# Kernel optimization log

Measured on AMD Instinct MI355X. Metric: run time of the kernel, lower is better.

The kernel has to match this reference:

```python
import jax, jax.numpy as jnp
import numpy as np

N_QUBITS = 4
N_LAYERS = 2
BATCH = 524288


def _apply_1q(state, U, wire, batched):
    """Apply a 2x2 gate U on `wire`. state: [B,2,2,2,2]; U: [B,2,2] if batched else [2,2]."""
    ax = wire + 1
    s = jnp.moveaxis(state, ax, 1)
    if batched:
        s = jnp.einsum('bij,bj...->bi...', U, s)
    else:
        s = jnp.einsum('ij,bj...->bi...', U, s)
    return jnp.moveaxis(s, 1, ax)


def _apply_cnot(state, control, target):
    cax, tax = control + 1, target + 1
    s0 = jnp.take(state, 0, axis=cax)
    s1 = jnp.take(state, 1, axis=cax)
    t_ax = tax - 1 if tax > cax else tax  # target axis after removing control axis
    s1 = jnp.flip(s1, axis=t_ax)
    return jnp.stack([s0, s1], axis=cax)


def _circuit(x, weight):
    B = x.shape[0]
    # Angle encoding: RY(tanh(x_i) * pi) per wire (per-sample angles)
    theta = jnp.tanh(x) * jnp.pi  # [B, 4]
    state = jnp.zeros((B,) + (2,) * N_QUBITS, jnp.complex64)
    state = state.at[(slice(None),) + (0,) * N_QUBITS].set(1.0)
    for q in range(N_QUBITS):
        h = theta[:, q] * 0.5
        c, s = jnp.cos(h), jnp.sin(h)
        Ury = jnp.stack([jnp.stack([c, -s], -1), jnp.stack([s, c], -1)], -2).astype(jnp.complex64)  # [B,2,2]
        state = _apply_1q(state, Ury, q, batched=True)
    for layer in range(N_LAYERS):
        for q in range(N_QUBITS):
            hy = weight[layer, q, 0] * 0.5
            cy, sy = jnp.cos(hy), jnp.sin(hy)
            Uy = jnp.stack([jnp.stack([cy, -sy]), jnp.stack([sy, cy])]).astype(jnp.complex64)
            state = _apply_1q(state, Uy, q, batched=False)
            hz = weight[layer, q, 1] * 0.5
            ez = jnp.exp(-1j * hz.astype(jnp.complex64))
            z0 = jnp.zeros((), jnp.complex64)
            Uz = jnp.stack([jnp.stack([ez, z0]), jnp.stack([z0, jnp.conj(ez)])])
            state = _apply_1q(state, Uz, q, batched=False)
        for q in range(N_QUBITS):
            state = _apply_cnot(state, q, (q + 1) % N_QUBITS)
    # <Z_i> = P(bit_i = 0) - P(bit_i = 1)
    probs = jnp.abs(state) ** 2  # [B,2,2,2,2] float32
    outs = []
    for q in range(N_QUBITS):
        other_axes = tuple(a for a in range(1, N_QUBITS + 1) if a != q + 1)
        marg = probs.sum(other_axes)  # [B,2]
        outs.append(marg[:, 0] - marg[:, 1])
    return jnp.stack(outs, axis=-1).astype(jnp.float32)  # [B,4]


def setup_inputs() -> dict:
    key = jax.random.key(0)
    kx, kw = jax.random.split(key)
    x = jax.random.normal(kx, (BATCH, N_QUBITS), dtype=jnp.float32)
    weight = jax.random.normal(kw, (N_LAYERS, N_QUBITS, 2), dtype=jnp.float32) * 0.1
    return {"x": x, "weight": weight}


def reference(x, weight):
    return _circuit(x, weight)
```

## Files before the change

kernel.cpp:

```cpp
#include <hip/hip_runtime.h>
#include <math.h>


#define HALF_PI_F 1.57079632679489661923f

__global__ __launch_bounds__(256) void build_C(
    const float* __restrict__ weight,
    float* __restrict__ C)
{
    __shared__ float cw[16], sw[16];
    __shared__ float Ur[16][16], Ui[16][16];
    __shared__ float A[4][16][16];

    if (threadIdx.x < 16) {
        float h = 0.5f * weight[threadIdx.x];
        __sincosf(h, &sw[threadIdx.x], &cw[threadIdx.x]);
    }
    __syncthreads();

    if (threadIdx.x < 16) {
        int col = threadIdx.x;
        float re[16], im[16];
        #pragma unroll
        for (int i = 0; i < 16; ++i) { re[i] = 0.f; im[i] = 0.f; }
        re[col] = 1.f;

        #pragma unroll
        for (int layer = 0; layer < 2; ++layer) {
            #pragma unroll
            for (int q = 0; q < 4; ++q) {
                float cy = cw[layer*8 + q*2 + 0];
                float sy = sw[layer*8 + q*2 + 0];
                float cz = cw[layer*8 + q*2 + 1];
                float sz = sw[layer*8 + q*2 + 1];
                int st = 8 >> q;
                #pragma unroll
                for (int i = 0; i < 16; ++i) {
                    if (i & st) continue;
                    int j = i | st;
                    float r0 = re[i], r1 = re[j], i0 = im[i], i1 = im[j];
                    float nr0 = cy*r0 - sy*r1;
                    float nr1 = sy*r0 + cy*r1;
                    float ni0 = cy*i0 - sy*i1;
                    float ni1 = sy*i0 + cy*i1;
                    re[i] = nr0*cz + ni0*sz;
                    im[i] = ni0*cz - nr0*sz;
                    re[j] = nr1*cz - ni1*sz;
                    im[j] = ni1*cz + nr1*sz;
                }
            }
            #pragma unroll
            for (int q = 0; q < 4; ++q) {
                int cb = 8 >> q;
                int tb = 8 >> ((q + 1) & 3);
                #pragma unroll
                for (int i = 0; i < 16; ++i) {
                    if ((i & cb) && !(i & tb)) {
                        int j = i | tb;
                        float tr = re[i]; re[i] = re[j]; re[j] = tr;
                        float ti = im[i]; im[i] = im[j]; im[j] = ti;
                    }
                }
            }
        }
        #pragma unroll
        for (int i = 0; i < 16; ++i) { Ur[i][col] = re[i]; Ui[i][col] = im[i]; }
    }
    __syncthreads();

    for (int e = threadIdx.x; e < 1024; e += 256) {
        int q = e >> 8, j = (e >> 4) & 15, k = e & 15;
        float sum = 0.f;
        for (int i = 0; i < 16; ++i) {
            float t = Ur[i][j]*Ur[i][k] + Ui[i][j]*Ui[i][k];
            sum += (i & (8 >> q)) ? -t : t;
        }
        A[q][j][k] = sum;
    }
    __syncthreads();

    for (int e = threadIdx.x; e < 400; e += 256) {
        int q = e / 100, pi = (e / 10) % 10, qi = e % 10;
        const int pu[10] = {0,0,0,0,1,1,1,2,2,3};
        const int pv[10] = {0,1,2,3,1,2,3,2,3,3};
        int u = pu[pi], v = pv[pi], r = pu[qi], s = pv[qi];
        float sum = 0.f;
        int a1s[2] = {u, v}, a2s[2] = {v, u};
        int b1s[2] = {r, s}, b2s[2] = {s, r};
        int na = (u == v) ? 1 : 2;
        int nb = (r == s) ? 1 : 2;
        for (int ia = 0; ia < na; ++ia)
            for (int ib = 0; ib < nb; ++ib)
                sum += A[q][a1s[ia]*4 + b1s[ib]][a2s[ia]*4 + b2s[ib]];
        C[e] = sum;
    }
}

__global__ __launch_bounds__(256) void qmain(
    const float* __restrict__ x,
    const float* __restrict__ C,
    float* __restrict__ out,
    int B)
{
    int tid = blockIdx.x * blockDim.x + threadIdx.x;
    if (tid >= B) return;

    float4 xv = reinterpret_cast<const float4*>(x)[tid];
    float xs[4] = {xv.x, xv.y, xv.z, xv.w};

    float c[4], s[4];
    #pragma unroll
    for (int q = 0; q < 4; ++q) {
        float e = __expf(2.f * xs[q]);
        float t = 1.f - __fdividef(2.f, e + 1.f);
        __sincosf(t * HALF_PI_F, &s[q], &c[q]);
    }

    float a4[4] = {c[0]*c[1], c[0]*s[1], s[0]*c[1], s[0]*s[1]};
    float b4[4] = {c[2]*c[3], c[2]*s[3], s[2]*c[3], s[2]*s[3]};

    const int pu[10] = {0,0,0,0,1,1,1,2,2,3};
    const int pv[10] = {0,1,2,3,1,2,3,2,3,3};
    float P[10], Q[10];
    #pragma unroll
    for (int i2 = 0; i2 < 10; ++i2) {
        P[i2] = a4[pu[i2]] * a4[pv[i2]];
        Q[i2] = b4[pu[i2]] * b4[pv[i2]];
    }

    float z[4];
    #pragma unroll
    for (int q = 0; q < 4; ++q) {
        float zq = 0.f;
        #pragma unroll
        for (int pi = 0; pi < 10; ++pi) {
            float t = 0.f;
            #pragma unroll
            for (int qi = 0; qi < 10; ++qi)
                t = fmaf(C[q*100 + pi*10 + qi], Q[qi], t);
            zq = fmaf(P[pi], t, zq);
        }
        z[q] = zq;
    }

    float4 o = {z[0], z[1], z[2], z[3]};
    reinterpret_cast<float4*>(out)[tid] = o;
}

extern "C" void kernel_launch(void* const* d_in, const int* in_sizes, int n_in,
                              void* d_out, int out_size, void* d_ws, size_t ws_size,
                              hipStream_t stream) {
    const float* x = (const float*)d_in[0];
    const float* w = (const float*)d_in[1];
    float* out = (float*)d_out;
    float* C = (float*)d_ws;
    int B = in_sizes[0] / 4;

    build_C<<<1, 256, 0, stream>>>(w, C);
    int block = 256;
    int grid = (B + block - 1) / block;
    qmain<<<grid, block, 0, stream>>>(x, C, out, B);
}
```

Baseline: 73.79 us.

## Fuse C-matrix build into main kernel, two samples per thread with packed math

```diff
diff --git a/kernel.cpp b/kernel.cpp
--- a/kernel.cpp
+++ b/kernel.cpp
@@ -4,71 +4,89 @@
 
 #define HALF_PI_F 1.57079632679489661923f
 
-__global__ __launch_bounds__(256) void build_C(
+typedef float f32x2 __attribute__((ext_vector_type(2)));
+
+__global__ __launch_bounds__(256) void qfused(
+    const float* __restrict__ x,
     const float* __restrict__ weight,
-    float* __restrict__ C)
+    float* __restrict__ out,
+    int B)
 {
     __shared__ float cw[16], sw[16];
     __shared__ float Ur[16][16], Ui[16][16];
     __shared__ float A[4][16][16];
+    __shared__ float4 C4[10][10];
 
-    if (threadIdx.x < 16) {
-        float h = 0.5f * weight[threadIdx.x];
-        __sincosf(h, &sw[threadIdx.x], &cw[threadIdx.x]);
+    const int tid = threadIdx.x;
+    const int s0 = blockIdx.x * 512 + tid;
+    const int s1 = s0 + 256;
+
+    float4 xv0 = (s0 < B) ? reinterpret_cast<const float4*>(x)[s0]
+                          : float4{0.f, 0.f, 0.f, 0.f};
+    float4 xv1 = (s1 < B) ? reinterpret_cast<const float4*>(x)[s1]
+                          : float4{0.f, 0.f, 0.f, 0.f};
+
+    if (tid < 16) {
+        float h = 0.5f * weight[tid];
+        __sincosf(h, &sw[tid], &cw[tid]);
     }
     __syncthreads();
 
-    if (threadIdx.x < 16) {
-        int col = threadIdx.x;
-        float re[16], im[16];
-        #pragma unroll
-        for (int i = 0; i < 16; ++i) { re[i] = 0.f; im[i] = 0.f; }
-        re[col] = 1.f;
+    {
+        const int wbase = (blockIdx.x & 3) * 64;
+        if (tid >= wbase && tid < wbase + 16) {
+            const int col = tid - wbase;
+            float re[16], im[16];
+            #pragma unroll
+            for (int i = 0; i < 16; ++i) { re[i] = 0.f; im[i] = 0.f; }
+            re[col] = 1.f;
 
-        #pragma unroll
-        for (int layer = 0; layer < 2; ++layer) {
             #pragma unroll
-            for (int q = 0; q < 4; ++q) {
-                float cy = cw[layer*8 + q*2 + 0];
-                float sy = sw[layer*8 + q*2 + 0];
-                float cz = cw[layer*8 + q*2 + 1];
-                float sz = sw[layer*8 + q*2 + 1];
-                int st = 8 >> q;
+            for (int layer = 0; layer < 2; ++layer) {
                 #pragma unroll
-                for (int i = 0; i < 16; ++i) {
-                    if (i & st) continue;
-                    int j = i | st;
-                    float r0 = re[i], r1 = re[j], i0 = im[i], i1 = im[j];
-                    float nr0 = cy*r0 - sy*r1;
-                    float nr1 = sy*r0 + cy*r1;
-                    float ni0 = cy*i0 - sy*i1;
-                    float ni1 = sy*i0 + cy*i1;
-                    re[i] = nr0*cz + ni0*sz;
-                    im[i] = ni0*cz - nr0*sz;
-                    re[j] = nr1*cz - ni1*sz;
-                    im[j] = ni1*cz + nr1*sz;
+                for (int q = 0; q < 4; ++q) {
+                    float cy = cw[layer*8 + q*2 + 0];
+                    float sy = sw[layer*8 + q*2 + 0];
+                    float cz = cw[layer*8 + q*2 + 1];
+                    float sz = sw[layer*8 + q*2 + 1];
+                    int st = 8 >> q;
+                    #pragma unroll
+                    for (int i = 0; i < 16; ++i) {
+                        if (i & st) continue;
+                        int j = i | st;
+                        float r0 = re[i], r1 = re[j], i0 = im[i], i1 = im[j];
+                        float nr0 = cy*r0 - sy*r1;
+                        float nr1 = sy*r0 + cy*r1;
+                        float ni0 = cy*i0 - sy*i1;
+                        float ni1 = sy*i0 + cy*i1;
+                        re[i] = nr0*cz + ni0*sz;
+                        im[i] = ni0*cz - nr0*sz;
+                        re[j] = nr1*cz - ni1*sz;
+                        im[j] = ni1*cz + nr1*sz;
+                    }
+                }
+                #pragma unroll
+                for (int q = 0; q < 4; ++q) {
+                    int cb = 8 >> q;
+                    int tb = 8 >> ((q + 1) & 3);
+                    #pragma unroll
+                    for (int i = 0; i < 16; ++i) {
+                        if ((i & cb) && !(i & tb)) {
+                            int j = i | tb;
+                            float tr = re[i]; re[i] = re[j]; re[j] = tr;
+                            float ti = im[i]; im[i] = im[j]; im[j] = ti;
+                        }
+                    }
                 }
             }
             #pragma unroll
-            for (int q = 0; q < 4; ++q) {
-                int cb = 8 >> q;
-                int tb = 8 >> ((q + 1) & 3);
-                #pragma unroll
-                for (int i = 0; i < 16; ++i) {
-                    if ((i & cb) && !(i & tb)) {
-                        int j = i | tb;
-                        float tr = re[i]; re[i] = re[j]; re[j] = tr;
-                        float ti = im[i]; im[i] = im[j]; im[j] = ti;
-                    }
-                }
-            }
+            for (int i = 0; i < 16; ++i) { Ur[i][col] = re[i]; Ui[i][col] = im[i]; }
         }
-        #pragma unroll
-        for (int i = 0; i < 16; ++i) { Ur[i][col] = re[i]; Ui[i][col] = im[i]; }
     }
     __syncthreads();
 
-    for (int e = threadIdx.x; e < 1024; e += 256) {
+    #pragma unroll
+    for (int e = tid; e < 1024; e += 256) {
         int q = e >> 8, j = (e >> 4) & 15, k = e & 15;
         float sum = 0.f;
         for (int i = 0; i < 16; ++i) {
@@ -79,72 +97,81 @@
     }
     __syncthreads();
 
-    for (int e = threadIdx.x; e < 400; e += 256) {
-        int q = e / 100, pi = (e / 10) % 10, qi = e % 10;
+    if (tid < 100) {
         const int pu[10] = {0,0,0,0,1,1,1,2,2,3};
         const int pv[10] = {0,1,2,3,1,2,3,2,3,3};
-        int u = pu[pi], v = pv[pi], r = pu[qi], s = pv[qi];
-        float sum = 0.f;
+        int pi = tid / 10, qi = tid % 10;
+        int u = pu[pi], v = pv[pi], r = pu[qi], sI = pv[qi];
         int a1s[2] = {u, v}, a2s[2] = {v, u};
-        int b1s[2] = {r, s}, b2s[2] = {s, r};
+        int b1s[2] = {r, sI}, b2s[2] = {sI, r};
         int na = (u == v) ? 1 : 2;
-        int nb = (r == s) ? 1 : 2;
+        int nb = (r == sI) ? 1 : 2;
+        float acc[4] = {0.f, 0.f, 0.f, 0.f};
         for (int ia = 0; ia < na; ++ia)
-            for (int ib = 0; ib < nb; ++ib)
-                sum += A[q][a1s[ia]*4 + b1s[ib]][a2s[ia]*4 + b2s[ib]];
-        C[e] = sum;
+            for (int ib = 0; ib < nb; ++ib) {
+                int j = a1s[ia]*4 + b1s[ib];
+                int k = a2s[ia]*4 + b2s[ib];
+                #pragma unroll
+                for (int q = 0; q < 4; ++q) acc[q] += A[q][j][k];
+            }
+        C4[pi][qi] = float4{acc[0], acc[1], acc[2], acc[3]};
     }
-}
-
-__global__ __launch_bounds__(256) void qmain(
-    const float* __restrict__ x,
-    const float* __restrict__ C,
-    float* __restrict__ out,
-    int B)
-{
-    int tid = blockIdx.x * blockDim.x + threadIdx.x;
-    if (tid >= B) return;
-
-    float4 xv = reinterpret_cast<const float4*>(x)[tid];
-    float xs[4] = {xv.x, xv.y, xv.z, xv.w};
-
-    float c[4], s[4];
-    #pragma unroll
-    for (int q = 0; q < 4; ++q) {
-        float e = __expf(2.f * xs[q]);
-        float t = 1.f - __fdividef(2.f, e + 1.f);
-        __sincosf(t * HALF_PI_F, &s[q], &c[q]);
-    }
-
-    float a4[4] = {c[0]*c[1], c[0]*s[1], s[0]*c[1], s[0]*s[1]};
-    float b4[4] = {c[2]*c[3], c[2]*s[3], s[2]*c[3], s[2]*s[3]};
+    __syncthreads();
 
     const int pu[10] = {0,0,0,0,1,1,1,2,2,3};
     const int pv[10] = {0,1,2,3,1,2,3,2,3,3};
-    float P[10], Q[10];
-    #pragma unroll
-    for (int i2 = 0; i2 < 10; ++i2) {
-        P[i2] = a4[pu[i2]] * a4[pv[i2]];
-        Q[i2] = b4[pu[i2]] * b4[pv[i2]];
+
+    float P0[10], Q0[10], P1[10], Q1[10];
+    {
+        float xs[8] = {xv0.x, xv0.y, xv0.z, xv0.w, xv1.x, xv1.y, xv1.z, xv1.w};
+        float c[8], s[8];
+        #pragma unroll
+        for (int q = 0; q < 8; ++q) {
+            float e = __expf(2.f * xs[q]);
+            float t = 1.f - __fdividef(2.f, e + 1.f);
+            __sincosf(t * HALF_PI_F, &s[q], &c[q]);
+        }
+        float a0[4] = {c[0]*c[1], c[0]*s[1], s[0]*c[1], s[0]*s[1]};
+        float b0[4] = {c[2]*c[3], c[2]*s[3], s[2]*c[3], s[2]*s[3]};
+        float a1[4] = {c[4]*c[5], c[4]*s[5], s[4]*c[5], s[4]*s[5]};
+        float b1[4] = {c[6]*c[7], c[6]*s[7], s[6]*c[7], s[6]*s[7]};
+        #pragma unroll
+        for (int i2 = 0; i2 < 10; ++i2) {
+            P0[i2] = a0[pu[i2]] * a0[pv[i2]];
+            Q0[i2] = b0[pu[i2]] * b0[pv[i2]];
+            P1[i2] = a1[pu[i2]] * a1[pv[i2]];
+            Q1[i2] = b1[pu[i2]] * b1[pv[i2]];
+        }
     }
 
-    float z[4];
+    f32x2 z01_0 = {0.f, 0.f}, z23_0 = {0.f, 0.f};
+    f32x2 z01_1 = {0.f, 0.f}, z23_1 = {0.f, 0.f};
     #pragma unroll
-    for (int q = 0; q < 4; ++q) {
-        float zq = 0.f;
+    for (int pi = 0; pi < 10; ++pi) {
+        f32x2 t01_0 = {0.f, 0.f}, t23_0 = {0.f, 0.f};
+        f32x2 t01_1 = {0.f, 0.f}, t23_1 = {0.f, 0.f};
         #pragma unroll
-        for (int pi = 0; pi < 10; ++pi) {
-            float t = 0.f;
-            #pragma unroll
-            for (int qi = 0; qi < 10; ++qi)
-                t = fmaf(C[q*100 + pi*10 + qi], Q[qi], t);
-            zq = fmaf(P[pi], t, zq);
+        for (int qi = 0; qi < 10; ++qi) {
+            float4 cv = C4[pi][qi];
+            f32x2 c01 = {cv.x, cv.y};
+            f32x2 c23 = {cv.z, cv.w};
+            f32x2 qb0 = {Q0[qi], Q0[qi]};
+            f32x2 qb1 = {Q1[qi], Q1[qi]};
+            t01_0 += c01 * qb0;  t23_0 += c23 * qb0;
+            t01_1 += c01 * qb1;  t23_1 += c23 * qb1;
         }
-        z[q] = zq;
+        f32x2 pb0 = {P0[pi], P0[pi]};
+        f32x2 pb1 = {P1[pi], P1[pi]};
+        z01_0 += t01_0 * pb0;  z23_0 += t23_0 * pb0;
+        z01_1 += t01_1 * pb1;  z23_1 += t23_1 * pb1;
     }
 
-    float4 o = {z[0], z[1], z[2], z[3]};
-    reinterpret_cast<float4*>(out)[tid] = o;
+    if (s0 < B)
+        reinterpret_cast<float4*>(out)[s0] =
+            float4{z01_0.x, z01_0.y, z23_0.x, z23_0.y};
+    if (s1 < B)
+        reinterpret_cast<float4*>(out)[s1] =
+            float4{z01_1.x, z01_1.y, z23_1.x, z23_1.y};
 }
 
 extern "C" void kernel_launch(void* const* d_in, const int* in_sizes, int n_in,
@@ -153,11 +180,7 @@
     const float* x = (const float*)d_in[0];
     const float* w = (const float*)d_in[1];
     float* out = (float*)d_out;
-    float* C = (float*)d_ws;
     int B = in_sizes[0] / 4;
-
-    build_C<<<1, 256, 0, stream>>>(w, C);
-    int block = 256;
-    int grid = (B + block - 1) / block;
-    qmain<<<grid, block, 0, stream>>>(x, C, out, B);
+    int grid = (B + 511) / 512;
+    qfused<<<grid, 256, 0, stream>>>(x, w, out, B);
 }
```

Result: slower. 104.6 us (+41.8%).
